# Optimization experiments

Hardware: AMD Instinct MI355X
Metric: run time of the kernel (lower is better)

The kernel has to match this reference:

```python
import jax, jax.numpy as jnp
import numpy as np

A, NA, D_OBS, B = 16, 8, 64, 128  # agents, actions, obs dim, graphs
DZ = D_OBS + NA  # obs_z_input_dim = 72


def _mlp(x, W1, b1, W2, b2):
    # Linear -> leaky_relu(0.01) -> Linear, torch Linear convention (y = x @ W.T + b)
    return jax.nn.leaky_relu(x @ W1.T + b1) @ W2.T + b2


def setup_inputs() -> dict:
    key = jax.random.key(0)
    ks = iter(jax.random.split(key, 40))
    p = {}
    p["obs"] = jax.random.normal(next(ks), (B * A, D_OBS), jnp.float32)
    p["policies"] = jax.random.uniform(next(ks), (B * A, NA), jnp.float32)
    p["actions"] = jax.random.uniform(next(ks), (B * A, NA), jnp.float32)

    def mk(name, inp, out):
        p[name + "_w"] = jax.random.normal(next(ks), (out, inp), jnp.float32) / np.sqrt(inp).astype(np.float32)
        p[name + "_b"] = jax.random.normal(next(ks), (out,), jnp.float32) * 0.01

    mk("kw1", D_OBS, 64); mk("kw2", 64, 64)   # key_weight layers
    mk("qw1", D_OBS, 64); mk("qw2", 64, 64)   # query_weight layers
    mk("ko1", DZ, 64);    mk("ko2", 64, 64)   # key_obsz layers
    mk("qo1", DZ, 64);    mk("qo2", 64, 64)   # query_obsz layers
    mk("av1", DZ, 64);    mk("av2", 64, 64)   # attention_value_obsz layers
    mk("fv1", 128, 64);   mk("fv2", 64, 8)    # final_value layers
    return p


def reference(obs, policies, actions,
              kw1_w, kw1_b, kw2_w, kw2_b, qw1_w, qw1_b, qw2_w, qw2_b,
              ko1_w, ko1_b, ko2_w, ko2_b, qo1_w, qo1_b, qo2_w, qo2_b,
              av1_w, av1_b, av2_w, av2_b, fv1_w, fv1_b, fv2_w, fv2_b):
    d_k_w = jnp.sqrt(jnp.float32(kw2_w.shape[0]))
    d_k_o = jnp.sqrt(jnp.float32(ko2_w.shape[0]))
    Bn = obs.shape[0] // A
    obs_b = obs.reshape(Bn, A, -1)                      # [B,A,Dobs]
    pi = policies.reshape(Bn, A, NA)
    act = actions.reshape(Bn, A, NA)

    # --- DGL update_all on the fully-connected (with self-loop) per-batch graph ---
    key_z = _mlp(obs_b, kw1_w, kw1_b, kw2_w, kw2_b)     # [B,A,dk]
    query_z = _mlp(obs_b, qw1_w, qw1_b, qw2_w, qw2_b)
    score = jnp.einsum('bjd,bid->bij', key_z, query_z)  # src key j -> dst query i
    w = jax.nn.sigmoid(score / d_k_w)[..., None]        # [B,A,A,1], mailbox gate
    z = w * act[:, None] + (1.0 - w) * pi[:, None]      # [B,A(i),A(j),NA]
    weight_z = w.reshape(Bn * A, A, 1)

    # obs_z[b,i,j] = cat(obs[b,j], z[b,i,j])
    obs_rep = jnp.broadcast_to(obs_b[:, None], (Bn, A, A, obs_b.shape[-1]))
    obs_z = jnp.concatenate([obs_rep, z], axis=-1)      # [B,A,A,DZ]

    diag = jnp.arange(A)
    src = obs_z[:, diag, diag]                          # source_obs_z_: [B,A,DZ] (j==i entry)

    key_o = _mlp(src, ko1_w, ko1_b, ko2_w, ko2_b)       # broadcast over j
    query_o = _mlp(obs_z, qo1_w, qo1_b, qo2_w, qo2_b)   # [B,A,A,dk]
    score_o = jnp.einsum('bid,bijd->bij', key_o, query_o)
    weights_o = jax.nn.softmax(jnp.exp(jnp.clip(score_o / d_k_o, -5.0, 5.0)), axis=-1)  # [B,A,A]

    # obs_z_pi[b,i,j,k] = op[b,j] if k==j else obs_z[b,i,k], op = cat(obs, pi)
    op = jnp.concatenate([obs_b, pi], axis=-1)          # [B,A,DZ]
    m = jnp.eye(A, dtype=obs.dtype)[None, None, :, :, None]          # (j,k) mask
    obs_z_pi = obs_z[:, :, None] * (1.0 - m) + op[:, None, None] * m  # [B,A,A,A,DZ]

    attn_src = _mlp(src, av1_w, av1_b, av2_w, av2_b)                  # [B,A,O]
    attn_other = _mlp(obs_z_pi, av1_w, av1_b, av2_w, av2_b)           # [B,A,A,A,O]

    w_exp = weights_o[:, None, :, :, None]              # [b,i,j,k,1] = weights_o[b,j,k]
    mixed = jnp.mean(attn_other * w_exp, axis=-2)       # mean over k -> [B,A,A,O]
    src_rep = jnp.broadcast_to(attn_src[:, None], mixed.shape)
    node_features = jnp.concatenate([src_rep, mixed], axis=-1)        # [B,A,A,2O]
    value = _mlp(node_features, fv1_w, fv1_b, fv2_w, fv2_b)           # [B,A,A,8]

    weights_obsz = jnp.broadcast_to(w_exp, (Bn, A, A, A, 1))
    return value, weight_z, weights_obsz
```

## Files before the change

### kernel.cpp

```cpp
#include <hip/hip_runtime.h>

#define A_ 16
#define NA_ 8
#define DOBS_ 64

typedef _Float16 f16;
typedef f16 h2 __attribute__((ext_vector_type(2)));
typedef f16 v8h __attribute__((ext_vector_type(8)));
typedef float v4f __attribute__((ext_vector_type(4)));

__device__ __forceinline__ float fdot2f(h2 a, h2 b, float c) {
  return __builtin_amdgcn_fdot2(a, b, c, false);
}
__device__ __forceinline__ float lrelu(float x) { return x > 0.f ? x : 0.01f * x; }

struct P {
  const float *obs, *pol, *act;
  const float *kw1w, *kw1b, *kw2w, *kw2b, *qw1w, *qw1b, *qw2w, *qw2b;
  const float *ko1w, *ko1b, *ko2w, *ko2b, *qo1w, *qo1b, *qo2w, *qo2b;
  const float *av1w, *av1b, *av2w, *av2b, *fv1w, *fv1b, *fv2w, *fv2b;
  float *out0, *out1, *out2;
  float *wsig, *wo;
};


#define SM_WQ0 0
#define SM_WQ1 4096
#define SM_S0 8192
#define SM_S1 9280
#define SM_S2 10368
#define SM_S3 11456
#define SM_OBS 12544
#define SM_GF2 13632
#define SM_WZ8 14656
#define SM_WSIG 15168
#define SM_WO 15424
#define SM_PI 15680
#define SM_ACT 15808
#define SM_C0 15936
#define SM_TOT 15952

__device__ __forceinline__ float dotWq(const float* Wq, const float* xrow, int o) {
  float a0 = 0.f, a1 = 0.f, a2 = 0.f, a3 = 0.f;
#pragma unroll
  for (int d4 = 0; d4 < 16; d4++) {
    const float4 w = ((const float4*)Wq)[d4 * 64 + o];
    const float4 x = *(const float4*)(xrow + 4 * d4);
    a0 += w.x * x.x; a1 += w.y * x.y; a2 += w.z * x.z; a3 += w.w * x.w;
  }
  return (a0 + a1) + (a2 + a3);
}

__global__ __launch_bounds__(1024) void critic_k1(P p) {
  __shared__ float sm[SM_TOT];
  const int tid = threadIdx.x;
  const int b = blockIdx.x;
  const int o = tid & 63, r = tid >> 6;

  const float4 Rkw1 = *(const float4*)(p.kw1w + o * 64 + 4 * r);
  const float4 Rqw1 = *(const float4*)(p.qw1w + o * 64 + 4 * r);
  const float4 Rkw2 = *(const float4*)(p.kw2w + o * 64 + 4 * r);
  const float4 Rqw2 = *(const float4*)(p.qw2w + o * 64 + 4 * r);
  const float4 Rko2 = *(const float4*)(p.ko2w + o * 64 + 4 * r);
  const float4 Rko1 = *(const float4*)(p.ko1w + o * 72 + 4 * r);
  const float4 Rqo1 = *(const float4*)(p.qo1w + o * 72 + 4 * r);
  const float4 Rkz0 = *(const float4*)(p.ko1w + o * 72 + 64);
  const float4 Rkz1 = *(const float4*)(p.ko1w + o * 72 + 68);
  float4 Rqo2;
  Rqo2.x = p.qo2w[(4 * r + 0) * 64 + o];
  Rqo2.y = p.qo2w[(4 * r + 1) * 64 + o];
  Rqo2.z = p.qo2w[(4 * r + 2) * 64 + o];
  Rqo2.w = p.qo2w[(4 * r + 3) * 64 + o];
  const float Bkw1 = p.kw1b[o], Bkw2 = p.kw2b[o], Bqw1 = p.qw1b[o], Bqw2 = p.qw2b[o];
  const float Bko1 = p.ko1b[o], Bko2 = p.ko2b[o], Bqo1 = p.qo1b[o], Bqo2v = p.qo2b[o];

  sm[SM_OBS + r * 68 + o] = p.obs[(size_t)b * 1024 + tid];
  if (tid < 128) sm[SM_PI + tid] = p.pol[(size_t)b * 128 + tid];
  else if (tid < 256) sm[SM_ACT + tid - 128] = p.act[(size_t)b * 128 + tid - 128];
  if (tid < 512) {
    const int oo = tid >> 3, c = tid & 7;
    sm[SM_WZ8 + (oo & 15) * 32 + (oo >> 4) * 8 + c] = p.qo1w[oo * 72 + 64 + c];
  }
  ((float4*)(sm + SM_WQ0))[tid] = Rkw1;
  ((float4*)(sm + SM_WQ1))[tid] = Rqw1;
  __syncthreads();

  {
    const float* xr = sm + SM_OBS + r * 68;
    sm[SM_S0 + r * 68 + o] = lrelu(dotWq(sm + SM_WQ0, xr, o) + Bkw1);
    sm[SM_S1 + r * 68 + o] = lrelu(dotWq(sm + SM_WQ1, xr, o) + Bqw1);
  }
  __syncthreads();
  ((float4*)(sm + SM_WQ0))[tid] = Rkw2;
  ((float4*)(sm + SM_WQ1))[tid] = Rqw2;
  __syncthreads();

  sm[SM_S2 + r * 68 + o] = dotWq(sm + SM_WQ0, sm + SM_S0 + r * 68, o) + Bkw2;
  sm[SM_S3 + r * 68 + o] = dotWq(sm + SM_WQ1, sm + SM_S1 + r * 68, o) + Bqw2;
  __syncthreads();
  ((float4*)(sm + SM_WQ0))[tid] = Rqo1;
  ((float4*)(sm + SM_WQ1))[tid] = Rko1;
  __syncthreads();

  {
    const float gv = dotWq(sm + SM_WQ0, sm + SM_OBS + r * 68, o) + Bqo1;
    sm[SM_GF2 + (o & 15) * 64 + r * 4 + (o >> 4)] = gv;
    const int j = (tid >> 2) & 15, g = tid & 3;
    float a0 = 0.f, a1 = 0.f, a2 = 0.f, a3 = 0.f;
#pragma unroll
    for (int t4 = 0; t4 < 4; t4++) {
      const float4 qv = *(const float4*)(sm + SM_S3 + r * 68 + g * 16 + 4 * t4);
      const float4 kv = *(const float4*)(sm + SM_S2 + j * 68 + g * 16 + 4 * t4);
      a0 += qv.x * kv.x; a1 += qv.y * kv.y; a2 += qv.z * kv.z; a3 += qv.w * kv.w;
    }
    float sc = (a0 + a1) + (a2 + a3);
    sc += __shfl_xor(sc, 1);
    sc += __shfl_xor(sc, 2);
    if (g == 0) {
      const float w = 1.f / (1.f + __expf(-sc * 0.125f));
      sm[SM_WSIG + r * 16 + j] = w;
      p.out1[(size_t)b * 256 + r * 16 + j] = w;
      p.wsig[(size_t)b * 256 + r * 16 + j] = w;
    }
  }
  __syncthreads();

  {
    float acc = dotWq(sm + SM_WQ1, sm + SM_OBS + r * 68, o) + Bko1;
    const float wrr = sm[SM_WSIG + r * 16 + r];
    const float* piR = sm + SM_PI + r * 8;
    const float* acR = sm + SM_ACT + r * 8;
    float z[8];
#pragma unroll
    for (int c = 0; c < 8; c++) z[c] = piR[c] + wrr * (acR[c] - piR[c]);
    acc += Rkz0.x * z[0] + Rkz0.y * z[1] + Rkz0.z * z[2] + Rkz0.w * z[3]
         + Rkz1.x * z[4] + Rkz1.y * z[5] + Rkz1.z * z[6] + Rkz1.w * z[7];
    sm[SM_S0 + r * 68 + o] = lrelu(acc);
    ((float4*)(sm + SM_WQ0))[tid] = Rko2;
  }
  __syncthreads();

  sm[SM_S1 + r * 68 + o] = dotWq(sm + SM_WQ0, sm + SM_S0 + r * 68, o) + Bko2;
  ((float4*)(sm + SM_WQ1))[tid] = Rqo2;
  __syncthreads();

  {
    sm[SM_S2 + r * 68 + o] = dotWq(sm + SM_WQ1, sm + SM_S1 + r * 68, o);
    float t = sm[SM_S1 + r * 68 + o] * Bqo2v;
#pragma unroll
    for (int mm = 1; mm < 64; mm <<= 1) t += __shfl_xor(t, mm);
    if (o == 0) sm[SM_C0 + r] = t;
  }
  __syncthreads();

  {
    const int j = (tid >> 2) & 15, g = tid & 3;
    const float wij = sm[SM_WSIG + r * 16 + j];
    const float* piR = sm + SM_PI + j * 8;
    const float* acR = sm + SM_ACT + j * 8;
    float z[8];
#pragma unroll
    for (int c = 0; c < 8; c++) z[c] = piR[c] + wij * (acR[c] - piR[c]);
    float sc = 0.f;
#pragma unroll
    for (int t = 0; t < 16; t++) {
      const float4 wa = *(const float4*)(sm + SM_WZ8 + t * 32 + g * 8);
      const float4 wb = *(const float4*)(sm + SM_WZ8 + t * 32 + g * 8 + 4);
      float hv = sm[SM_GF2 + t * 64 + j * 4 + g]
        + wa.x * z[0] + wa.y * z[1] + wa.z * z[2] + wa.w * z[3]
        + wb.x * z[4] + wb.y * z[5] + wb.z * z[6] + wb.w * z[7];
      hv = lrelu(hv);
      sc += sm[SM_S2 + r * 68 + g * 16 + t] * hv;
    }
    sc += __shfl_xor(sc, 1);
    sc += __shfl_xor(sc, 2);
    if (g == 0) {
      float yv = (sc + sm[SM_C0 + r]) * 0.125f;
      yv = fminf(fmaxf(yv, -5.f), 5.f);
      sm[SM_S3 + r * 16 + j] = __expf(yv);
    }
  }
  __syncthreads();

  if (tid < 256) {
    const int i = tid >> 4, j = tid & 15;
    const float* e = sm + SM_S3;
    float m = -1e30f;
#pragma unroll
    for (int jj = 0; jj < 16; jj++) m = fmaxf(m, e[i * 16 + jj]);
    float den = 0.f;
#pragma unroll
    for (int jj = 0; jj < 16; jj++) den += __expf(e[i * 16 + jj] - m);
    const float val = __expf(e[i * 16 + j] - m) / den;
    sm[SM_WO + i * 16 + j] = val;
    p.wo[(size_t)b * 256 + tid] = val;
  }
  __syncthreads();
  {
    const int q = tid >> 2, g = tid & 3, k = q & 15;
    *(float4*)(p.out2 + ((size_t)b * 256 + q) * 16 + 4 * g) =
        *(const float4*)(sm + SM_WO + k * 16 + 4 * g);
  }
}


struct alignas(16) SMem2 {
  f16 obsH[16][72];
  f16 AOsrcD[16 * 72];
  f16 APT[64 * 24];
  f16 AextH[16 * 40];
  f16 fv2pw[8 * 64];
  f16 slice[8][1536];
  union {
    struct { f16 av1H[64 * 96]; f16 av2H[64 * 72]; } av;
    f16 fv1H[64 * 136];
  } W;
  float pi[16][8], act[16][8], wsig[16][16];
  float av1b[64], av2b[64], fv1b[64], fv2b[8];
};

__device__ __forceinline__ v8h bfrag(const f16* Wm, int stride, int nt, int ks, int lane) {
  const int n = lane & 15, q = lane >> 4;
  return *(const v8h*)(Wm + (nt * 16 + n) * stride + ks * 32 + q * 8);
}

__device__ __forceinline__ void av_mlp(const SMem2& s, f16* Hbuf, v8h az, int lane, v4f acc2[4]) {
  const int m = lane & 15, q = lane >> 4;
  const v8h a0 = *(const v8h*)(&s.obsH[m][q * 8]);
  const v8h a1 = *(const v8h*)(&s.obsH[m][32 + q * 8]);
#pragma unroll
  for (int nt = 0; nt < 4; nt++) {
    const float bv = s.av1b[nt * 16 + m];
    v4f acc = {bv, bv, bv, bv};
    acc = __builtin_amdgcn_mfma_f32_16x16x32_f16(a0, bfrag(s.W.av.av1H, 96, nt, 0, lane), acc, 0, 0, 0);
    acc = __builtin_amdgcn_mfma_f32_16x16x32_f16(a1, bfrag(s.W.av.av1H, 96, nt, 1, lane), acc, 0, 0, 0);
    acc = __builtin_amdgcn_mfma_f32_16x16x32_f16(az, bfrag(s.W.av.av1H, 96, nt, 2, lane), acc, 0, 0, 0);
#pragma unroll
    for (int reg = 0; reg < 4; reg++)
      Hbuf[(q * 4 + reg) * 72 + nt * 16 + m] = (f16)lrelu(acc[reg]);
  }
  const v8h h0 = *(const v8h*)(Hbuf + m * 72 + q * 8);
  const v8h h1 = *(const v8h*)(Hbuf + m * 72 + 32 + q * 8);
#pragma unroll
  for (int nt = 0; nt < 4; nt++) {
    const float bv = s.av2b[nt * 16 + m];
    v4f acc = {bv, bv, bv, bv};
    acc = __builtin_amdgcn_mfma_f32_16x16x32_f16(h0, bfrag(s.W.av.av2H, 72, nt, 0, lane), acc, 0, 0, 0);
    acc = __builtin_amdgcn_mfma_f32_16x16x32_f16(h1, bfrag(s.W.av.av2H, 72, nt, 1, lane), acc, 0, 0, 0);
    acc2[nt] = acc;
  }
}

__global__ __launch_bounds__(512) void critic_k2(P p) {
  __shared__ SMem2 s;
  const int tid = threadIdx.x;
  const int b = blockIdx.x >> 1, ibase = (blockIdx.x & 1) * 8;
  const int w = tid >> 6, lane = tid & 63;
  const int m = lane & 15, quad = lane >> 4;
  const int i = ibase + w;

  float4 rfv[4];
#pragma unroll
  for (int qq = 0; qq < 4; qq++) rfv[qq] = ((const float4*)p.fv1w)[tid * 4 + qq];

  for (int k = tid; k < 1024; k += 512) s.obsH[k >> 6][k & 63] = (f16)p.obs[(size_t)b * 1024 + k];
  if (tid < 128) { s.pi[tid >> 3][tid & 7] = p.pol[(size_t)b * 128 + tid]; }
  else if (tid < 256) { int k = tid - 128; s.act[k >> 3][k & 7] = p.act[(size_t)b * 128 + k]; }
  for (int k = tid; k < 256; k += 512) s.wsig[k >> 4][k & 15] = p.wsig[(size_t)b * 256 + k];
  {
    const int kk = tid >> 5, j2 = tid & 31;
    float v = 0.f;
    if (j2 < 16) v = p.wo[(size_t)b * 256 + kk * 16 + j2] * 0.0625f;
    else if (j2 - 16 == kk) v = p.wo[(size_t)b * 256 + kk * 16 + kk] * 0.0625f;
    s.AextH[kk * 40 + j2] = (f16)v;
  }
  {
    const int row = tid >> 3, c0 = (tid & 7) * 9;
#pragma unroll
    for (int c = 0; c < 9; c++) s.W.av.av1H[row * 96 + c0 + c] = (f16)p.av1w[row * 72 + c0 + c];
  }
  {
    const int row = tid >> 3, c0 = 72 + (tid & 7) * 3;
#pragma unroll
    for (int c = 0; c < 3; c++) s.W.av.av1H[row * 96 + c0 + c] = (f16)0.f;
  }
  for (int k = tid; k < 4096; k += 512) s.W.av.av2H[(k >> 6) * 72 + (k & 63)] = (f16)p.av2w[k];
  s.fv2pw[tid] = (f16)p.fv2w[tid];
  if (tid < 64) { s.av1b[tid] = p.av1b[tid]; s.av2b[tid] = p.av2b[tid]; s.fv1b[tid] = p.fv1b[tid]; }
  else if (tid < 72) s.fv2b[tid - 64] = p.fv2b[tid - 64];
  __syncthreads();

  f16* Sl = &s.slice[w][0];
  {
    v8h az = {};
    if (quad == 0) {
      const float wv = s.wsig[i][m];
#pragma unroll
      for (int c = 0; c < 8; c++) az[c] = (f16)(s.pi[m][c] + wv * (s.act[m][c] - s.pi[m][c]));
    }
    v4f acc2[4];
    av_mlp(s, Sl, az, lane, acc2);
#pragma unroll
    for (int nt = 0; nt < 4; nt++)
#pragma unroll
      for (int reg = 0; reg < 4; reg++)
        Sl[(nt * 16 + m) * 24 + quad * 4 + reg] = (f16)acc2[nt][reg];
  }
  if (w == 0) {
    v8h az = {};
    if (quad == 0) {
#pragma unroll
      for (int c = 0; c < 8; c++) az[c] = (f16)s.pi[m][c];
    }
    v4f acc2[4];
    av_mlp(s, s.APT, az, lane, acc2);
#pragma unroll
    for (int nt = 0; nt < 4; nt++)
#pragma unroll
      for (int reg = 0; reg < 4; reg++)
        s.APT[(nt * 16 + m) * 24 + quad * 4 + reg] = (f16)acc2[nt][reg];
  }
  if (w == 1) {
    v8h az = {};
    if (quad == 0) {
      const float wv = s.wsig[m][m];
#pragma unroll
      for (int c = 0; c < 8; c++) az[c] = (f16)(s.pi[m][c] + wv * (s.act[m][c] - s.pi[m][c]));
    }
    v4f acc2[4];
    av_mlp(s, s.AOsrcD, az, lane, acc2);
#pragma unroll
    for (int nt = 0; nt < 4; nt++)
#pragma unroll
      for (int reg = 0; reg < 4; reg++)
        s.AOsrcD[(quad * 4 + reg) * 72 + nt * 16 + m] = (f16)acc2[nt][reg];
  }
  __syncthreads();

#pragma unroll
  for (int qq = 0; qq < 4; qq++) {
    const int e0 = tid * 16 + qq * 4;
    h2* d = (h2*)&s.W.fv1H[(e0 >> 7) * 136 + (e0 & 127)];
    d[0] = h2{(f16)rfv[qq].x, (f16)rfv[qq].y};
    d[1] = h2{(f16)rfv[qq].z, (f16)rfv[qq].w};
  }
  __syncthreads();

  {
    const v8h am = *(const v8h*)(&s.AextH[m * 40 + quad * 8]);
    v4f macc[4];
#pragma unroll
    for (int nt = 0; nt < 4; nt++) {
      const int o = nt * 16 + m;
      v8h bf;
      if (quad < 2) {
        bf = *(const v8h*)(Sl + o * 24 + quad * 8);
      } else {
        const v8h apv = *(const v8h*)(&s.APT[o * 24 + (quad - 2) * 8]);
        const v8h aov = *(const v8h*)(Sl + o * 24 + (quad - 2) * 8);
        bf = apv - aov;
      }
      v4f z4 = {0.f, 0.f, 0.f, 0.f};
      macc[nt] = __builtin_amdgcn_mfma_f32_16x16x32_f16(am, bf, z4, 0, 0, 0);
    }
#pragma unroll
    for (int nt = 0; nt < 4; nt++)
#pragma unroll
      for (int reg = 0; reg < 4; reg++)
        Sl[(quad * 4 + reg) * 72 + nt * 16 + m] = (f16)macc[nt][reg];
  }

  {
    const v8h f0 = *(const v8h*)(&s.AOsrcD[m * 72 + quad * 8]);
    const v8h f1 = *(const v8h*)(&s.AOsrcD[m * 72 + 32 + quad * 8]);
    const v8h f2 = *(const v8h*)(Sl + m * 72 + quad * 8);
    const v8h f3 = *(const v8h*)(Sl + m * 72 + 32 + quad * 8);
#pragma unroll
    for (int nt = 0; nt < 4; nt++) {
      const float bv = s.fv1b[nt * 16 + m];
      v4f acc = {bv, bv, bv, bv};
      acc = __builtin_amdgcn_mfma_f32_16x16x32_f16(f0, bfrag(s.W.fv1H, 136, nt, 0, lane), acc, 0, 0, 0);
      acc = __builtin_amdgcn_mfma_f32_16x16x32_f16(f1, bfrag(s.W.fv1H, 136, nt, 1, lane), acc, 0, 0, 0);
      acc = __builtin_amdgcn_mfma_f32_16x16x32_f16(f2, bfrag(s.W.fv1H, 136, nt, 2, lane), acc, 0, 0, 0);
      acc = __builtin_amdgcn_mfma_f32_16x16x32_f16(f3, bfrag(s.W.fv1H, 136, nt, 3, lane), acc, 0, 0, 0);
#pragma unroll
      for (int reg = 0; reg < 4; reg++)
        Sl[(quad * 4 + reg) * 72 + nt * 16 + m] = (f16)lrelu(acc[reg]);
    }
  }
  {
    const int g2 = quad;
    float y0 = s.fv2b[2 * g2], y1 = s.fv2b[2 * g2 + 1];
#pragma unroll
    for (int o2 = 0; o2 < 32; o2++) {
      const h2 hh = *(const h2*)(Sl + m * 72 + 2 * o2);
      const h2 w0 = *(const h2*)(&s.fv2pw[(2 * g2) * 64 + 2 * o2]);
      const h2 w1 = *(const h2*)(&s.fv2pw[(2 * g2 + 1) * 64 + 2 * o2]);
      y0 = fdot2f(w0, hh, y0);
      y1 = fdot2f(w1, hh, y1);
    }
    *(float2*)(p.out0 + ((size_t)b * 256 + i * 16 + m) * 8 + 2 * g2) = make_float2(y0, y1);
  }
}

extern "C" void kernel_launch(void* const* d_in, const int* in_sizes, int n_in,
                              void* d_out, int out_size, void* d_ws, size_t ws_size,
                              hipStream_t stream) {
  P p;
  p.obs = (const float*)d_in[0];
  p.pol = (const float*)d_in[1];
  p.act = (const float*)d_in[2];
  p.kw1w = (const float*)d_in[3];  p.kw1b = (const float*)d_in[4];
  p.kw2w = (const float*)d_in[5];  p.kw2b = (const float*)d_in[6];
  p.qw1w = (const float*)d_in[7];  p.qw1b = (const float*)d_in[8];
  p.qw2w = (const float*)d_in[9];  p.qw2b = (const float*)d_in[10];
  p.ko1w = (const float*)d_in[11]; p.ko1b = (const float*)d_in[12];
  p.ko2w = (const float*)d_in[13]; p.ko2b = (const float*)d_in[14];
  p.qo1w = (const float*)d_in[15]; p.qo1b = (const float*)d_in[16];
  p.qo2w = (const float*)d_in[17]; p.qo2b = (const float*)d_in[18];
  p.av1w = (const float*)d_in[19]; p.av1b = (const float*)d_in[20];
  p.av2w = (const float*)d_in[21]; p.av2b = (const float*)d_in[22];
  p.fv1w = (const float*)d_in[23]; p.fv1b = (const float*)d_in[24];
  p.fv2w = (const float*)d_in[25]; p.fv2b = (const float*)d_in[26];

  const int Bn = in_sizes[0] / (A_ * DOBS_);
  p.out0 = (float*)d_out;
  p.out1 = p.out0 + (size_t)Bn * A_ * A_ * NA_;
  p.out2 = p.out1 + (size_t)Bn * A_ * A_;
  p.wsig = (float*)d_ws;
  p.wo = p.wsig + (size_t)Bn * 256;

  hipLaunchKernelGGL(critic_k1, dim3(Bn), dim3(1024), 0, stream, p);
  hipLaunchKernelGGL(critic_k2, dim3(2 * Bn), dim3(512), 0, stream, p);
}
```

Baseline: 134.8 us.

## Move critic_k1 per-agent MLPs to split-fp16 MFMA and vectorize k2 weight loads

Replaces the scalar fp32 dot-product layers in the first kernel with 16x16x32 fp16 MFMA tiles. Activations and weights are split into high and low fp16 parts so the result stays close to fp32 accuracy. All seven 64-wide layers now run on four waves through one shared weight buffer, with a barrier between phases. The second kernel also prefetches the av1 and av2 weights into registers with float4 loads instead of strided scalar global loads. The cost is six MFMAs per tile plus the extra conversion work and barriers, while twelve of sixteen waves sit idle during each GEMM.

```diff
diff --git a/kernel.cpp b/kernel.cpp
--- a/kernel.cpp
+++ b/kernel.cpp
@@ -24,182 +24,259 @@
 };
 
 
-#define SM_WQ0 0
-#define SM_WQ1 4096
-#define SM_S0 8192
-#define SM_S1 9280
-#define SM_S2 10368
-#define SM_S3 11456
-#define SM_OBS 12544
-#define SM_GF2 13632
-#define SM_WZ8 14656
-#define SM_WSIG 15168
-#define SM_WO 15424
-#define SM_PI 15680
-#define SM_ACT 15808
-#define SM_C0 15936
-#define SM_TOT 15952
-
-__device__ __forceinline__ float dotWq(const float* Wq, const float* xrow, int o) {
-  float a0 = 0.f, a1 = 0.f, a2 = 0.f, a3 = 0.f;
-#pragma unroll
-  for (int d4 = 0; d4 < 16; d4++) {
-    const float4 w = ((const float4*)Wq)[d4 * 64 + o];
-    const float4 x = *(const float4*)(xrow + 4 * d4);
-    a0 += w.x * x.x; a1 += w.y * x.y; a2 += w.z * x.z; a3 += w.w * x.w;
-  }
-  return (a0 + a1) + (a2 + a3);
+struct alignas(16) SM1 {
+  f16 WAh[64 * 72], WAl[64 * 72];
+  f16 obsh[16 * 72], obsl[16 * 72];
+  f16 X1h[16 * 72], X1l[16 * 72];
+  f16 X2h[16 * 72], X2l[16 * 72];
+  float S2[16 * 68], S3[16 * 68];
+  float G2[16 * 68];
+  float wz[512];
+  float bias8[8 * 64];
+  float pi[128], act[128], wsig[256], wo[256], c0[16], e[256];
+};
+
+__device__ __forceinline__ v4f gemm_tile(const f16* Xh, const f16* Xl,
+                                         const f16* Wh, const f16* Wl,
+                                         float bv, int nt, int lane) {
+  const int m = lane & 15, q = lane >> 4;
+  v4f acc = {bv, bv, bv, bv};
+  const v8h ah0 = *(const v8h*)(Xh + m * 72 + q * 8);
+  const v8h ah1 = *(const v8h*)(Xh + m * 72 + 32 + q * 8);
+  const v8h al0 = *(const v8h*)(Xl + m * 72 + q * 8);
+  const v8h al1 = *(const v8h*)(Xl + m * 72 + 32 + q * 8);
+  const f16* wr = Wh + (nt * 16 + m) * 72 + q * 8;
+  const v8h bh0 = *(const v8h*)(wr);
+  const v8h bh1 = *(const v8h*)(wr + 32);
+  const f16* wr2 = Wl + (nt * 16 + m) * 72 + q * 8;
+  const v8h bl0 = *(const v8h*)(wr2);
+  const v8h bl1 = *(const v8h*)(wr2 + 32);
+  acc = __builtin_amdgcn_mfma_f32_16x16x32_f16(ah0, bh0, acc, 0, 0, 0);
+  acc = __builtin_amdgcn_mfma_f32_16x16x32_f16(ah1, bh1, acc, 0, 0, 0);
+  acc = __builtin_amdgcn_mfma_f32_16x16x32_f16(ah0, bl0, acc, 0, 0, 0);
+  acc = __builtin_amdgcn_mfma_f32_16x16x32_f16(ah1, bl1, acc, 0, 0, 0);
+  acc = __builtin_amdgcn_mfma_f32_16x16x32_f16(al0, bh0, acc, 0, 0, 0);
+  acc = __builtin_amdgcn_mfma_f32_16x16x32_f16(al1, bh1, acc, 0, 0, 0);
+  return acc;
+}
+
+__device__ __forceinline__ void writeX(f16* Xh, f16* Xl, v4f acc, int nt, int lane, bool relu) {
+  const int m = lane & 15, q = lane >> 4;
+#pragma unroll
+  for (int reg = 0; reg < 4; reg++) {
+    float y = acc[reg];
+    if (relu) y = lrelu(y);
+    const f16 yh = (f16)y;
+    Xh[(q * 4 + reg) * 72 + nt * 16 + m] = yh;
+    Xl[(q * 4 + reg) * 72 + nt * 16 + m] = (f16)(y - (float)yh);
+  }
+}
+
+__device__ __forceinline__ void putW(f16* Wh, f16* Wl, float4 v, int o, int r) {
+  h2* dh = (h2*)(Wh + o * 72 + 4 * r);
+  h2* dl = (h2*)(Wl + o * 72 + 4 * r);
+  const f16 hx = (f16)v.x, hy = (f16)v.y, hz = (f16)v.z, hw = (f16)v.w;
+  dh[0] = h2{hx, hy};
+  dh[1] = h2{hz, hw};
+  dl[0] = h2{(f16)(v.x - (float)hx), (f16)(v.y - (float)hy)};
+  dl[1] = h2{(f16)(v.z - (float)hz), (f16)(v.w - (float)hw)};
 }
 
 __global__ __launch_bounds__(1024) void critic_k1(P p) {
-  __shared__ float sm[SM_TOT];
+  __shared__ SM1 s;
   const int tid = threadIdx.x;
   const int b = blockIdx.x;
   const int o = tid & 63, r = tid >> 6;
+  const int w = r, lane = tid & 63, m = lane & 15, quad = lane >> 4;
 
   const float4 Rkw1 = *(const float4*)(p.kw1w + o * 64 + 4 * r);
+  const float4 Rkw2 = *(const float4*)(p.kw2w + o * 64 + 4 * r);
   const float4 Rqw1 = *(const float4*)(p.qw1w + o * 64 + 4 * r);
-  const float4 Rkw2 = *(const float4*)(p.kw2w + o * 64 + 4 * r);
   const float4 Rqw2 = *(const float4*)(p.qw2w + o * 64 + 4 * r);
   const float4 Rko2 = *(const float4*)(p.ko2w + o * 64 + 4 * r);
   const float4 Rko1 = *(const float4*)(p.ko1w + o * 72 + 4 * r);
   const float4 Rqo1 = *(const float4*)(p.qo1w + o * 72 + 4 * r);
-  const float4 Rkz0 = *(const float4*)(p.ko1w + o * 72 + 64);
-  const float4 Rkz1 = *(const float4*)(p.ko1w + o * 72 + 68);
   float4 Rqo2;
   Rqo2.x = p.qo2w[(4 * r + 0) * 64 + o];
   Rqo2.y = p.qo2w[(4 * r + 1) * 64 + o];
   Rqo2.z = p.qo2w[(4 * r + 2) * 64 + o];
   Rqo2.w = p.qo2w[(4 * r + 3) * 64 + o];
-  const float Bkw1 = p.kw1b[o], Bkw2 = p.kw2b[o], Bqw1 = p.qw1b[o], Bqw2 = p.qw2b[o];
-  const float Bko1 = p.ko1b[o], Bko2 = p.ko2b[o], Bqo1 = p.qo1b[o], Bqo2v = p.qo2b[o];
-
-  sm[SM_OBS + r * 68 + o] = p.obs[(size_t)b * 1024 + tid];
-  if (tid < 128) sm[SM_PI + tid] = p.pol[(size_t)b * 128 + tid];
-  else if (tid < 256) sm[SM_ACT + tid - 128] = p.act[(size_t)b * 128 + tid - 128];
+  const float Bqo2v = p.qo2b[o];
+  float Rwzqo = 0.f;
+  if (tid < 512) Rwzqo = p.qo1w[(tid >> 3) * 72 + 64 + (tid & 7)];
+
   if (tid < 512) {
-    const int oo = tid >> 3, c = tid & 7;
-    sm[SM_WZ8 + (oo & 15) * 32 + (oo >> 4) * 8 + c] = p.qo1w[oo * 72 + 64 + c];
-  }
-  ((float4*)(sm + SM_WQ0))[tid] = Rkw1;
-  ((float4*)(sm + SM_WQ1))[tid] = Rqw1;
-  __syncthreads();
-
-  {
-    const float* xr = sm + SM_OBS + r * 68;
-    sm[SM_S0 + r * 68 + o] = lrelu(dotWq(sm + SM_WQ0, xr, o) + Bkw1);
-    sm[SM_S1 + r * 68 + o] = lrelu(dotWq(sm + SM_WQ1, xr, o) + Bqw1);
-  }
-  __syncthreads();
-  ((float4*)(sm + SM_WQ0))[tid] = Rkw2;
-  ((float4*)(sm + SM_WQ1))[tid] = Rqw2;
-  __syncthreads();
-
-  sm[SM_S2 + r * 68 + o] = dotWq(sm + SM_WQ0, sm + SM_S0 + r * 68, o) + Bkw2;
-  sm[SM_S3 + r * 68 + o] = dotWq(sm + SM_WQ1, sm + SM_S1 + r * 68, o) + Bqw2;
-  __syncthreads();
-  ((float4*)(sm + SM_WQ0))[tid] = Rqo1;
-  ((float4*)(sm + SM_WQ1))[tid] = Rko1;
-  __syncthreads();
-
-  {
-    const float gv = dotWq(sm + SM_WQ0, sm + SM_OBS + r * 68, o) + Bqo1;
-    sm[SM_GF2 + (o & 15) * 64 + r * 4 + (o >> 4)] = gv;
+    const float2 ov = ((const float2*)(p.obs + (size_t)b * 1024))[tid];
+    const int e0 = 2 * tid, r0 = e0 >> 6, c0 = e0 & 63;
+    const f16 hx = (f16)ov.x, hy = (f16)ov.y;
+    *(h2*)(s.obsh + r0 * 72 + c0) = h2{hx, hy};
+    *(h2*)(s.obsl + r0 * 72 + c0) = h2{(f16)(ov.x - (float)hx), (f16)(ov.y - (float)hy)};
+  }
+  if (tid < 128) s.pi[tid] = p.pol[(size_t)b * 128 + tid];
+  else if (tid < 256) s.act[tid - 128] = p.act[(size_t)b * 128 + tid - 128];
+  if (tid < 64) {
+    s.bias8[tid] = p.kw1b[tid];        s.bias8[64 + tid] = p.kw2b[tid];
+    s.bias8[128 + tid] = p.qw1b[tid];  s.bias8[192 + tid] = p.qw2b[tid];
+    s.bias8[256 + tid] = p.ko1b[tid];  s.bias8[320 + tid] = p.ko2b[tid];
+    s.bias8[384 + tid] = p.qo1b[tid];
+  }
+  if (tid < 512) s.wz[tid] = p.ko1w[(tid >> 3) * 72 + 64 + (tid & 7)];
+  putW(s.WAh, s.WAl, Rkw1, o, r);
+  __syncthreads();
+
+  if (w < 4) {
+    v4f a = gemm_tile(s.obsh, s.obsl, s.WAh, s.WAl, s.bias8[w * 16 + m], w, lane);
+    writeX(s.X1h, s.X1l, a, w, lane, true);
+  }
+  __syncthreads();
+  putW(s.WAh, s.WAl, Rkw2, o, r);
+  __syncthreads();
+  if (w < 4) {
+    v4f a = gemm_tile(s.X1h, s.X1l, s.WAh, s.WAl, s.bias8[64 + w * 16 + m], w, lane);
+#pragma unroll
+    for (int reg = 0; reg < 4; reg++) s.S2[(quad * 4 + reg) * 68 + w * 16 + m] = a[reg];
+  }
+  __syncthreads();
+  putW(s.WAh, s.WAl, Rqw1, o, r);
+  __syncthreads();
+  if (w < 4) {
+    v4f a = gemm_tile(s.obsh, s.obsl, s.WAh, s.WAl, s.bias8[128 + w * 16 + m], w, lane);
+    writeX(s.X2h, s.X2l, a, w, lane, true);
+  }
+  __syncthreads();
+  putW(s.WAh, s.WAl, Rqw2, o, r);
+  __syncthreads();
+  if (w < 4) {
+    v4f a = gemm_tile(s.X2h, s.X2l, s.WAh, s.WAl, s.bias8[192 + w * 16 + m], w, lane);
+#pragma unroll
+    for (int reg = 0; reg < 4; reg++) s.S3[(quad * 4 + reg) * 68 + w * 16 + m] = a[reg];
+  }
+  __syncthreads();
+
+  {
     const int j = (tid >> 2) & 15, g = tid & 3;
     float a0 = 0.f, a1 = 0.f, a2 = 0.f, a3 = 0.f;
 #pragma unroll
     for (int t4 = 0; t4 < 4; t4++) {
-      const float4 qv = *(const float4*)(sm + SM_S3 + r * 68 + g * 16 + 4 * t4);
-      const float4 kv = *(const float4*)(sm + SM_S2 + j * 68 + g * 16 + 4 * t4);
+      const float4 qv = *(const float4*)(s.S3 + r * 68 + g * 16 + 4 * t4);
+      const float4 kv = *(const float4*)(s.S2 + j * 68 + g * 16 + 4 * t4);
       a0 += qv.x * kv.x; a1 += qv.y * kv.y; a2 += qv.z * kv.z; a3 += qv.w * kv.w;
     }
     float sc = (a0 + a1) + (a2 + a3);
     sc += __shfl_xor(sc, 1);
     sc += __shfl_xor(sc, 2);
     if (g == 0) {
-      const float w = 1.f / (1.f + __expf(-sc * 0.125f));
-      sm[SM_WSIG + r * 16 + j] = w;
-      p.out1[(size_t)b * 256 + r * 16 + j] = w;
-      p.wsig[(size_t)b * 256 + r * 16 + j] = w;
-    }
-  }
-  __syncthreads();
-
-  {
-    float acc = dotWq(sm + SM_WQ1, sm + SM_OBS + r * 68, o) + Bko1;
-    const float wrr = sm[SM_WSIG + r * 16 + r];
-    const float* piR = sm + SM_PI + r * 8;
-    const float* acR = sm + SM_ACT + r * 8;
+      const float wv = 1.f / (1.f + __expf(-sc * 0.125f));
+      s.wsig[r * 16 + j] = wv;
+      p.out1[(size_t)b * 256 + r * 16 + j] = wv;
+      p.wsig[(size_t)b * 256 + r * 16 + j] = wv;
+    }
+    putW(s.WAh, s.WAl, Rko1, o, r);
+  }
+  __syncthreads();
+
+  if (w < 4) {
+    v4f a = gemm_tile(s.obsh, s.obsl, s.WAh, s.WAl, s.bias8[256 + w * 16 + m], w, lane);
+    const int oo = w * 16 + m;
+    float wzv[8];
+    *(float4*)wzv = *(const float4*)(s.wz + oo * 8);
+    *(float4*)(wzv + 4) = *(const float4*)(s.wz + oo * 8 + 4);
+#pragma unroll
+    for (int reg = 0; reg < 4; reg++) {
+      const int rr = quad * 4 + reg;
+      const float wrr = s.wsig[rr * 16 + rr];
+      float zp = 0.f;
+#pragma unroll
+      for (int c = 0; c < 8; c++) {
+        const float zc = s.pi[rr * 8 + c] + wrr * (s.act[rr * 8 + c] - s.pi[rr * 8 + c]);
+        zp += wzv[c] * zc;
+      }
+      const float y = lrelu(a[reg] + zp);
+      const f16 yh = (f16)y;
+      s.X2h[rr * 72 + oo] = yh;
+      s.X2l[rr * 72 + oo] = (f16)(y - (float)yh);
+    }
+  }
+  __syncthreads();
+  putW(s.WAh, s.WAl, Rko2, o, r);
+  __syncthreads();
+  if (w < 4) {
+    v4f a = gemm_tile(s.X2h, s.X2l, s.WAh, s.WAl, s.bias8[320 + w * 16 + m], w, lane);
+    writeX(s.X1h, s.X1l, a, w, lane, false);
+  }
+  __syncthreads();
+  putW(s.WAh, s.WAl, Rqo2, o, r);
+  __syncthreads();
+  if (w < 4) {
+    v4f a = gemm_tile(s.X1h, s.X1l, s.WAh, s.WAl, 0.f, w, lane);
+#pragma unroll
+    for (int reg = 0; reg < 4; reg++) s.S2[(quad * 4 + reg) * 68 + w * 16 + m] = a[reg];
+  }
+  {
+    const float kv = (float)s.X1h[r * 72 + o] + (float)s.X1l[r * 72 + o];
+    float t = kv * Bqo2v;
+#pragma unroll
+    for (int mm = 1; mm < 64; mm <<= 1) t += __shfl_xor(t, mm);
+    if (o == 0) s.c0[r] = t;
+  }
+  __syncthreads();
+  putW(s.WAh, s.WAl, Rqo1, o, r);
+  if (tid < 512) {
+    const int oo = tid >> 3, c = tid & 7;
+    s.wz[(oo & 15) * 32 + (oo >> 4) * 8 + c] = Rwzqo;
+  }
+  __syncthreads();
+  if (w < 4) {
+    v4f a = gemm_tile(s.obsh, s.obsl, s.WAh, s.WAl, s.bias8[384 + w * 16 + m], w, lane);
+#pragma unroll
+    for (int reg = 0; reg < 4; reg++) s.G2[m * 68 + (quad * 4 + reg) * 4 + w] = a[reg];
+  }
+  __syncthreads();
+
+  {
+    const int j = (tid >> 2) & 15, g = tid & 3;
+    const float wij = s.wsig[r * 16 + j];
     float z[8];
 #pragma unroll
-    for (int c = 0; c < 8; c++) z[c] = piR[c] + wrr * (acR[c] - piR[c]);
-    acc += Rkz0.x * z[0] + Rkz0.y * z[1] + Rkz0.z * z[2] + Rkz0.w * z[3]
-         + Rkz1.x * z[4] + Rkz1.y * z[5] + Rkz1.z * z[6] + Rkz1.w * z[7];
-    sm[SM_S0 + r * 68 + o] = lrelu(acc);
-    ((float4*)(sm + SM_WQ0))[tid] = Rko2;
-  }
-  __syncthreads();
-
-  sm[SM_S1 + r * 68 + o] = dotWq(sm + SM_WQ0, sm + SM_S0 + r * 68, o) + Bko2;
-  ((float4*)(sm + SM_WQ1))[tid] = Rqo2;
-  __syncthreads();
-
-  {
-    sm[SM_S2 + r * 68 + o] = dotWq(sm + SM_WQ1, sm + SM_S1 + r * 68, o);
-    float t = sm[SM_S1 + r * 68 + o] * Bqo2v;
-#pragma unroll
-    for (int mm = 1; mm < 64; mm <<= 1) t += __shfl_xor(t, mm);
-    if (o == 0) sm[SM_C0 + r] = t;
-  }
-  __syncthreads();
-
-  {
-    const int j = (tid >> 2) & 15, g = tid & 3;
-    const float wij = sm[SM_WSIG + r * 16 + j];
-    const float* piR = sm + SM_PI + j * 8;
-    const float* acR = sm + SM_ACT + j * 8;
-    float z[8];
-#pragma unroll
-    for (int c = 0; c < 8; c++) z[c] = piR[c] + wij * (acR[c] - piR[c]);
+    for (int c = 0; c < 8; c++) z[c] = s.pi[j * 8 + c] + wij * (s.act[j * 8 + c] - s.pi[j * 8 + c]);
     float sc = 0.f;
 #pragma unroll
     for (int t = 0; t < 16; t++) {
-      const float4 wa = *(const float4*)(sm + SM_WZ8 + t * 32 + g * 8);
-      const float4 wb = *(const float4*)(sm + SM_WZ8 + t * 32 + g * 8 + 4);
-      float hv = sm[SM_GF2 + t * 64 + j * 4 + g]
+      const float4 wa = *(const float4*)(s.wz + t * 32 + g * 8);
+      const float4 wb = *(const float4*)(s.wz + t * 32 + g * 8 + 4);
+      float hv = s.G2[t * 68 + j * 4 + g]
         + wa.x * z[0] + wa.y * z[1] + wa.z * z[2] + wa.w * z[3]
         + wb.x * z[4] + wb.y * z[5] + wb.z * z[6] + wb.w * z[7];
       hv = lrelu(hv);
-      sc += sm[SM_S2 + r * 68 + g * 16 + t] * hv;
+      sc += s.S2[r * 68 + g * 16 + t] * hv;
     }
     sc += __shfl_xor(sc, 1);
     sc += __shfl_xor(sc, 2);
     if (g == 0) {
-      float yv = (sc + sm[SM_C0 + r]) * 0.125f;
+      float yv = (sc + s.c0[r]) * 0.125f;
       yv = fminf(fmaxf(yv, -5.f), 5.f);
-      sm[SM_S3 + r * 16 + j] = __expf(yv);
+      s.e[r * 16 + j] = __expf(yv);
     }
   }
   __syncthreads();
 
   if (tid < 256) {
     const int i = tid >> 4, j = tid & 15;
-    const float* e = sm + SM_S3;
-    float m = -1e30f;
-#pragma unroll
-    for (int jj = 0; jj < 16; jj++) m = fmaxf(m, e[i * 16 + jj]);
+    float mx = -1e30f;
+#pragma unroll
+    for (int jj = 0; jj < 16; jj++) mx = fmaxf(mx, s.e[i * 16 + jj]);
     float den = 0.f;
 #pragma unroll
-    for (int jj = 0; jj < 16; jj++) den += __expf(e[i * 16 + jj] - m);
-    const float val = __expf(e[i * 16 + j] - m) / den;
-    sm[SM_WO + i * 16 + j] = val;
+    for (int jj = 0; jj < 16; jj++) den += __expf(s.e[i * 16 + jj] - mx);
+    const float val = __expf(s.e[i * 16 + j] - mx) / den;
+    s.wo[i * 16 + j] = val;
     p.wo[(size_t)b * 256 + tid] = val;
   }
   __syncthreads();
   {
     const int q = tid >> 2, g = tid & 3, k = q & 15;
     *(float4*)(p.out2 + ((size_t)b * 256 + q) * 16 + 4 * g) =
-        *(const float4*)(sm + SM_WO + k * 16 + 4 * g);
+        *(const float4*)(s.wo + k * 16 + 4 * g);
   }
 }
 
@@ -262,6 +339,11 @@
   float4 rfv[4];
 #pragma unroll
   for (int qq = 0; qq < 4; qq++) rfv[qq] = ((const float4*)p.fv1w)[tid * 4 + qq];
+  const float4 rav1a = ((const float4*)p.av1w)[tid * 2];
+  const float4 rav1b = ((const float4*)p.av1w)[tid * 2 + 1];
+  const float rav1c = p.av1w[4096 + tid];
+  const float4 rav2a = ((const float4*)p.av2w)[tid * 2];
+  const float4 rav2b = ((const float4*)p.av2w)[tid * 2 + 1];
 
   for (int k = tid; k < 1024; k += 512) s.obsH[k >> 6][k & 63] = (f16)p.obs[(size_t)b * 1024 + k];
   if (tid < 128) { s.pi[tid >> 3][tid & 7] = p.pol[(size_t)b * 128 + tid]; }
@@ -275,16 +357,28 @@
     s.AextH[kk * 40 + j2] = (f16)v;
   }
   {
-    const int row = tid >> 3, c0 = (tid & 7) * 9;
-#pragma unroll
-    for (int c = 0; c < 9; c++) s.W.av.av1H[row * 96 + c0 + c] = (f16)p.av1w[row * 72 + c0 + c];
+    float av1v[8] = {rav1a.x, rav1a.y, rav1a.z, rav1a.w, rav1b.x, rav1b.y, rav1b.z, rav1b.w};
+#pragma unroll
+    for (int e = 0; e < 8; e++) {
+      const int k = tid * 8 + e, rr = k / 72, cc = k - rr * 72;
+      s.W.av.av1H[rr * 96 + cc] = (f16)av1v[e];
+    }
+    const int k = 4096 + tid, rr = k / 72, cc = k - rr * 72;
+    s.W.av.av1H[rr * 96 + cc] = (f16)rav1c;
   }
   {
     const int row = tid >> 3, c0 = 72 + (tid & 7) * 3;
 #pragma unroll
     for (int c = 0; c < 3; c++) s.W.av.av1H[row * 96 + c0 + c] = (f16)0.f;
   }
-  for (int k = tid; k < 4096; k += 512) s.W.av.av2H[(k >> 6) * 72 + (k & 63)] = (f16)p.av2w[k];
+  {
+    float av2v[8] = {rav2a.x, rav2a.y, rav2a.z, rav2a.w, rav2b.x, rav2b.y, rav2b.z, rav2b.w};
+#pragma unroll
+    for (int e = 0; e < 8; e++) {
+      const int k = tid * 8 + e;
+      s.W.av.av2H[(k >> 6) * 72 + (k & 63)] = (f16)av2v[e];
+    }
+  }
   s.fv2pw[tid] = (f16)p.fv2w[tid];
   if (tid < 64) { s.av1b[tid] = p.av1b[tid]; s.av2b[tid] = p.av2b[tid]; s.fv1b[tid] = p.fv1b[tid]; }
   else if (tid < 72) s.fv2b[tid - 64] = p.fv2b[tid - 64];
```

New measurement: 130.4 us. 3.2% less time.
